# Kernel optimization log

Measured on AMD Instinct MI355X. Metric: run time of the kernel, lower is better.

The kernel has to match this reference:

```python
import jax, jax.numpy as jnp
import numpy as np

IALPHA = 0.95
ITAU = 8.0


def setup_inputs() -> dict:
    key = jax.random.key(0)
    kx, = jax.random.split(key, 1)
    B, H, W, C = 32, 512, 512, 4
    x = jax.random.normal(kx, (B, H, W, C), dtype=jnp.float32)
    alpha = jnp.full((1,), IALPHA, dtype=jnp.float32)
    tau = jnp.full((1,), ITAU, dtype=jnp.float32)
    return {"x": x, "alpha": alpha, "tau": tau}


def reference(x, alpha, tau):
    # x: [B, H, W, C] (NHWC), alpha/tau: [1] learned scalars
    B, H, W, C = x.shape
    L = H * W
    # per (batch, channel) row of L pixels, sorted descending (tf.math.top_k k=L)
    xr = jnp.transpose(x, (0, 3, 1, 2)).reshape(B * C, L)  # [B*C, L]
    s = -jnp.sort(-xr, axis=1)  # descending sort
    st = s[:, int(0.99 * L)]  # low order statistic (near min)
    en = s[:, int(0.01 * L)]  # high order statistic (near max)
    th0 = st + (en - st) * alpha[0]  # [B*C]
    th = th0.reshape(B, C)[:, None, None, :]  # broadcast to [B, H, W, C]
    th = jnp.broadcast_to(th, (B, H, W, C))
    val0 = (th > 1e-14).astype(x.dtype)
    th = th * val0
    val_st = th + (1.0 - val0)  # avoid div-by-zero where threshold is tiny
    tau_m = tau[0] / val_st
    # proxtype == 3: relu(x) * sigmoid(tau * (|x| - th))
    return jax.nn.relu(x) * jax.nn.sigmoid(tau_m * (jnp.abs(x) - th))
```

## Files before the change

### kernel.cpp

```cpp
#include <hip/hip_runtime.h>
#include <math.h>


#define HW_POS   (512 * 512)
#define NPOS     (32 * HW_POS)
#define NBINS    2048
#define NROWS    128
#define K_ST     2621
#define K_EN     259522
#define POS_PER_BLOCK 8192
#define HIST_BLOCKS (NPOS / POS_PER_BLOCK)

typedef float nfloat4 __attribute__((ext_vector_type(4)));

__global__ void zero_hist(int4* ws) {
    int idx = blockIdx.x * blockDim.x + threadIdx.x;
    ws[idx] = make_int4(0, 0, 0, 0);
}

__device__ __forceinline__ void hist4(const float4 v, int* lh) {
    int b0 = (int)fminf(fmaxf((v.x + 4.0f) * 256.0f, 0.0f), 2047.0f);
    int b1 = (int)fminf(fmaxf((v.y + 4.0f) * 256.0f, 0.0f), 2047.0f);
    int b2 = (int)fminf(fmaxf((v.z + 4.0f) * 256.0f, 0.0f), 2047.0f);
    int b3 = (int)fminf(fmaxf((v.w + 4.0f) * 256.0f, 0.0f), 2047.0f);
    atomicAdd(&lh[0 * NBINS + b0], 1);
    atomicAdd(&lh[1 * NBINS + b1], 1);
    atomicAdd(&lh[2 * NBINS + b2], 1);
    atomicAdd(&lh[3 * NBINS + b3], 1);
}

__global__ __launch_bounds__(256) void hist_kernel(const float4* __restrict__ x,
                                                   int* __restrict__ rowHist) {
    __shared__ int lh[4 * NBINS];
    const int tid = threadIdx.x;
    for (int i = tid; i < 4 * NBINS; i += 256) lh[i] = 0;
    __syncthreads();

    const int base = blockIdx.x * POS_PER_BLOCK;
    const int row0 = (base >> 18) * 4;
    const float4* xp = x + base + tid;

    for (int i = 0; i < POS_PER_BLOCK / 256; i += 4) {
        float4 v0 = xp[(i + 0) * 256];
        float4 v1 = xp[(i + 1) * 256];
        float4 v2 = xp[(i + 2) * 256];
        float4 v3 = xp[(i + 3) * 256];
        hist4(v0, lh);
        hist4(v1, lh);
        hist4(v2, lh);
        hist4(v3, lh);
    }
    __syncthreads();

    for (int i = tid; i < 4 * NBINS; i += 256) {
        int v = lh[i];
        if (v) atomicAdd(&rowHist[(row0 + (i >> 11)) * NBINS + (i & (NBINS - 1))], v);
    }
}

__global__ __launch_bounds__(64) void select_kernel(const int* __restrict__ rowHist,
                                                    const float* __restrict__ alpha,
                                                    const float* __restrict__ tau,
                                                    float* __restrict__ thArr,
                                                    float* __restrict__ taumArr) {
    const int row  = blockIdx.x;
    const int lane = threadIdx.x;
    const int* h   = rowHist + row * NBINS;

    int vals[32];
    int local = 0;
    #pragma unroll
    for (int j = 0; j < 32; ++j) { vals[j] = h[lane * 32 + j]; local += vals[j]; }

    int incl = local;
    #pragma unroll
    for (int off = 1; off < 64; off <<= 1) {
        int n = __shfl_up(incl, off, 64);
        if (lane >= off) incl += n;
    }
    int run = incl - local;

    int binSt = 1 << 20, binEn = 1 << 20;
    #pragma unroll
    for (int j = 0; j < 32; ++j) {
        run += vals[j];
        int b = lane * 32 + j;
        if (run >= K_ST + 1 && binSt == (1 << 20)) binSt = b;
        if (run >= K_EN + 1 && binEn == (1 << 20)) binEn = b;
    }
    #pragma unroll
    for (int off = 32; off; off >>= 1) {
        binSt = min(binSt, __shfl_down(binSt, off, 64));
        binEn = min(binEn, __shfl_down(binEn, off, 64));
    }

    if (lane == 0) {
        float st = -4.0f + ((float)binSt + 0.5f) * (1.0f / 256.0f);
        float en = -4.0f + ((float)binEn + 0.5f) * (1.0f / 256.0f);
        float a  = alpha[0];
        float th0 = st + (en - st) * a;
        bool  v0  = th0 > 1e-14f;
        float th  = v0 ? th0 : 0.0f;
        float vst = v0 ? th0 : 1.0f;
        thArr[row]   = th;
        taumArr[row] = tau[0] / vst;
    }
}

__device__ __forceinline__ float prox1(float v, float th, float tm) {
    float r = fmaxf(v, 0.0f);
    float z = tm * (fabsf(v) - th);
    return r / (1.0f + __expf(-z));
}

__global__ __launch_bounds__(256) void out_kernel(const float4* __restrict__ x,
                                                  const float4* __restrict__ thArr,
                                                  const float4* __restrict__ taumArr,
                                                  float4* __restrict__ out) {
    int idx    = blockIdx.x * blockDim.x + threadIdx.x;
    int stride = gridDim.x * blockDim.x;
    for (int p = idx; p < NPOS; p += stride) {
        int b = p >> 18;
        float4 v  = x[p];
        float4 t4 = thArr[b];
        float4 m4 = taumArr[b];
        nfloat4 o;
        o.x = prox1(v.x, t4.x, m4.x);
        o.y = prox1(v.y, t4.y, m4.y);
        o.z = prox1(v.z, t4.z, m4.z);
        o.w = prox1(v.w, t4.w, m4.w);
        __builtin_nontemporal_store(o, (nfloat4*)&out[p]);
    }
}

extern "C" void kernel_launch(void* const* d_in, const int* in_sizes, int n_in,
                              void* d_out, int out_size, void* d_ws, size_t ws_size,
                              hipStream_t stream) {
    const float* x     = (const float*)d_in[0];
    const float* alpha = (const float*)d_in[1];
    const float* tau   = (const float*)d_in[2];
    float*       out   = (float*)d_out;

    int*   rowHist = (int*)d_ws;
    float* thArr   = (float*)((char*)d_ws + NROWS * NBINS * 4);
    float* taumArr = thArr + NROWS;

    zero_hist<<<256, 256, 0, stream>>>((int4*)rowHist);
    hist_kernel<<<HIST_BLOCKS, 256, 0, stream>>>((const float4*)x, rowHist);
    select_kernel<<<NROWS, 64, 0, stream>>>(rowHist, alpha, tau, thArr, taumArr);
    out_kernel<<<4096, 256, 0, stream>>>((const float4*)x, (const float4*)thArr,
                                         (const float4*)taumArr, (float4*)out);
}
```

Measured before the change: 272.9 us.

## Fuse threshold selection into histogram kernel via last-block counter

Folds the per-row threshold selection into the histogram kernel: every block increments a global counter, and the last block to finish scans all 128 row histograms with four waves. This removes one kernel launch, at the cost of running the selection serially in a single block. The histogram loop now issues eight loads before binning instead of four. The output kernel now uses one block per 1024 positions and loads the per-batch thresholds once per block instead of once per element, replacing the grid-stride loop.

New measurement: 522.7 us. +91.5%, slower.

```diff
diff --git a/kernel.cpp b/kernel.cpp
--- a/kernel.cpp
+++ b/kernel.cpp
@@ -13,9 +13,14 @@
 
 typedef float nfloat4 __attribute__((ext_vector_type(4)));
 
-__global__ void zero_hist(int4* ws) {
+#define WS_CTR_OFF   (NROWS * NBINS * 4)
+#define WS_TH_OFF    (WS_CTR_OFF + 64)
+#define WS_TAUM_OFF  (WS_TH_OFF + NROWS * 4)
+
+__global__ void zero_hist(int4* ws, int* ctr) {
     int idx = blockIdx.x * blockDim.x + threadIdx.x;
     ws[idx] = make_int4(0, 0, 0, 0);
+    if (idx == 0) *ctr = 0;
 }
 
 __device__ __forceinline__ void hist4(const float4 v, int* lh) {
@@ -30,8 +35,14 @@
 }
 
 __global__ __launch_bounds__(256) void hist_kernel(const float4* __restrict__ x,
-                                                   int* __restrict__ rowHist) {
+                                                   int* __restrict__ rowHist,
+                                                   int* __restrict__ ctr,
+                                                   const float* __restrict__ alpha,
+                                                   const float* __restrict__ tau,
+                                                   float* __restrict__ thArr,
+                                                   float* __restrict__ taumArr) {
     __shared__ int lh[4 * NBINS];
+    __shared__ int lastFlag;
     const int tid = threadIdx.x;
     for (int i = tid; i < 4 * NBINS; i += 256) lh[i] = 0;
     __syncthreads();
@@ -40,15 +51,12 @@
     const int row0 = (base >> 18) * 4;
     const float4* xp = x + base + tid;
 
-    for (int i = 0; i < POS_PER_BLOCK / 256; i += 4) {
-        float4 v0 = xp[(i + 0) * 256];
-        float4 v1 = xp[(i + 1) * 256];
-        float4 v2 = xp[(i + 2) * 256];
-        float4 v3 = xp[(i + 3) * 256];
-        hist4(v0, lh);
-        hist4(v1, lh);
-        hist4(v2, lh);
-        hist4(v3, lh);
+    for (int i = 0; i < POS_PER_BLOCK / 256; i += 8) {
+        float4 v[8];
+        #pragma unroll
+        for (int j = 0; j < 8; ++j) v[j] = xp[(i + j) * 256];
+        #pragma unroll
+        for (int j = 0; j < 8; ++j) hist4(v[j], lh);
     }
     __syncthreads();
 
@@ -56,54 +64,59 @@
         int v = lh[i];
         if (v) atomicAdd(&rowHist[(row0 + (i >> 11)) * NBINS + (i & (NBINS - 1))], v);
     }
-}
 
-__global__ __launch_bounds__(64) void select_kernel(const int* __restrict__ rowHist,
-                                                    const float* __restrict__ alpha,
-                                                    const float* __restrict__ tau,
-                                                    float* __restrict__ thArr,
-                                                    float* __restrict__ taumArr) {
-    const int row  = blockIdx.x;
-    const int lane = threadIdx.x;
-    const int* h   = rowHist + row * NBINS;
+    __threadfence();
+    __syncthreads();
+    if (tid == 0) lastFlag = (atomicAdd(ctr, 1) == HIST_BLOCKS - 1);
+    __syncthreads();
+    if (!lastFlag) return;
+    __threadfence();
 
-    int vals[32];
-    int local = 0;
-    #pragma unroll
-    for (int j = 0; j < 32; ++j) { vals[j] = h[lane * 32 + j]; local += vals[j]; }
+    const int lane = tid & 63, wave = tid >> 6;
+    for (int it = 0; it < NROWS / 4; ++it) {
+        const int row = it * 4 + wave;
+        const int* h = rowHist + row * NBINS;
 
-    int incl = local;
-    #pragma unroll
-    for (int off = 1; off < 64; off <<= 1) {
-        int n = __shfl_up(incl, off, 64);
-        if (lane >= off) incl += n;
-    }
-    int run = incl - local;
+        int vals[32];
+        int local = 0;
+        #pragma unroll
+        for (int j = 0; j < 32; ++j) {
+            vals[j] = __hip_atomic_load(&h[lane * 32 + j], __ATOMIC_RELAXED,
+                                        __HIP_MEMORY_SCOPE_AGENT);
+            local += vals[j];
+        }
 
-    int binSt = 1 << 20, binEn = 1 << 20;
-    #pragma unroll
-    for (int j = 0; j < 32; ++j) {
-        run += vals[j];
-        int b = lane * 32 + j;
-        if (run >= K_ST + 1 && binSt == (1 << 20)) binSt = b;
-        if (run >= K_EN + 1 && binEn == (1 << 20)) binEn = b;
-    }
-    #pragma unroll
-    for (int off = 32; off; off >>= 1) {
-        binSt = min(binSt, __shfl_down(binSt, off, 64));
-        binEn = min(binEn, __shfl_down(binEn, off, 64));
-    }
+        int incl = local;
+        #pragma unroll
+        for (int off = 1; off < 64; off <<= 1) {
+            int n = __shfl_up(incl, off, 64);
+            if (lane >= off) incl += n;
+        }
+        int run = incl - local;
 
-    if (lane == 0) {
-        float st = -4.0f + ((float)binSt + 0.5f) * (1.0f / 256.0f);
-        float en = -4.0f + ((float)binEn + 0.5f) * (1.0f / 256.0f);
-        float a  = alpha[0];
-        float th0 = st + (en - st) * a;
-        bool  v0  = th0 > 1e-14f;
-        float th  = v0 ? th0 : 0.0f;
-        float vst = v0 ? th0 : 1.0f;
-        thArr[row]   = th;
-        taumArr[row] = tau[0] / vst;
+        int binSt = 1 << 20, binEn = 1 << 20;
+        #pragma unroll
+        for (int j = 0; j < 32; ++j) {
+            run += vals[j];
+            int b = lane * 32 + j;
+            if (run >= K_ST + 1 && binSt == (1 << 20)) binSt = b;
+            if (run >= K_EN + 1 && binEn == (1 << 20)) binEn = b;
+        }
+        #pragma unroll
+        for (int off = 32; off; off >>= 1) {
+            binSt = min(binSt, __shfl_down(binSt, off, 64));
+            binEn = min(binEn, __shfl_down(binEn, off, 64));
+        }
+
+        if (lane == 0) {
+            float st = -4.0f + ((float)binSt + 0.5f) * (1.0f / 256.0f);
+            float en = -4.0f + ((float)binEn + 0.5f) * (1.0f / 256.0f);
+            float a  = alpha[0];
+            float th0 = st + (en - st) * a;
+            bool  v0  = th0 > 1e-14f;
+            thArr[row]   = v0 ? th0 : 0.0f;
+            taumArr[row] = tau[0] / (v0 ? th0 : 1.0f);
+        }
     }
 }
 
@@ -117,19 +130,20 @@
                                                   const float4* __restrict__ thArr,
                                                   const float4* __restrict__ taumArr,
                                                   float4* __restrict__ out) {
-    int idx    = blockIdx.x * blockDim.x + threadIdx.x;
-    int stride = gridDim.x * blockDim.x;
-    for (int p = idx; p < NPOS; p += stride) {
-        int b = p >> 18;
-        float4 v  = x[p];
-        float4 t4 = thArr[b];
-        float4 m4 = taumArr[b];
+    const int blk  = blockIdx.x;
+    const int b    = blk >> 8;
+    const float4 t4 = thArr[b];
+    const float4 m4 = taumArr[b];
+    const int base = blk * 1024 + threadIdx.x;
+    #pragma unroll
+    for (int k = 0; k < 4; ++k) {
+        float4 v = x[base + k * 256];
         nfloat4 o;
         o.x = prox1(v.x, t4.x, m4.x);
         o.y = prox1(v.y, t4.y, m4.y);
         o.z = prox1(v.z, t4.z, m4.z);
         o.w = prox1(v.w, t4.w, m4.w);
-        __builtin_nontemporal_store(o, (nfloat4*)&out[p]);
+        __builtin_nontemporal_store(o, (nfloat4*)&out[base + k * 256]);
     }
 }
 
@@ -142,12 +156,13 @@
     float*       out   = (float*)d_out;
 
     int*   rowHist = (int*)d_ws;
-    float* thArr   = (float*)((char*)d_ws + NROWS * NBINS * 4);
-    float* taumArr = thArr + NROWS;
+    int*   ctr     = (int*)((char*)d_ws + WS_CTR_OFF);
+    float* thArr   = (float*)((char*)d_ws + WS_TH_OFF);
+    float* taumArr = (float*)((char*)d_ws + WS_TAUM_OFF);
 
-    zero_hist<<<256, 256, 0, stream>>>((int4*)rowHist);
-    hist_kernel<<<HIST_BLOCKS, 256, 0, stream>>>((const float4*)x, rowHist);
-    select_kernel<<<NROWS, 64, 0, stream>>>(rowHist, alpha, tau, thArr, taumArr);
-    out_kernel<<<4096, 256, 0, stream>>>((const float4*)x, (const float4*)thArr,
-                                         (const float4*)taumArr, (float4*)out);
+    zero_hist<<<256, 256, 0, stream>>>((int4*)rowHist, ctr);
+    hist_kernel<<<HIST_BLOCKS, 256, 0, stream>>>((const float4*)x, rowHist, ctr,
+                                                 alpha, tau, thArr, taumArr);
+    out_kernel<<<NPOS / 1024, 256, 0, stream>>>((const float4*)x, (const float4*)thArr,
+                                                (const float4*)taumArr, (float4*)out);
 }
```
